# Performance work log

Measured on AMD Instinct MI355X. Metric: run time of the kernel, lower is better.

Reference implementation:

```python
import jax, jax.numpy as jnp
import numpy as np

D_MODEL = 1024
NUM_HEADS = 16
HEAD_DIM = D_MODEL // NUM_HEADS
B, S = 4, 2048


def setup_inputs() -> dict:
    key = jax.random.key(0)
    ks = jax.random.split(key, 12)
    s = 1.0 / np.sqrt(D_MODEL)
    return {
        "inputs_q": jax.random.normal(ks[0], (B, S, D_MODEL), jnp.float32),
        "inputs_k": jax.random.normal(ks[1], (B, S, D_MODEL), jnp.float32),
        "inputs_v": jax.random.normal(ks[2], (B, S, D_MODEL), jnp.float32),
        "Wq": jax.random.normal(ks[3], (D_MODEL, D_MODEL), jnp.float32) * s,
        "bq": jax.random.normal(ks[4], (D_MODEL,), jnp.float32) * 0.01,
        "Wk": jax.random.normal(ks[5], (D_MODEL, D_MODEL), jnp.float32) * s,
        "bk": jax.random.normal(ks[6], (D_MODEL,), jnp.float32) * 0.01,
        "Wv": jax.random.normal(ks[7], (D_MODEL, D_MODEL), jnp.float32) * s,
        "bv": jax.random.normal(ks[8], (D_MODEL,), jnp.float32) * 0.01,
        "Wo": jax.random.normal(ks[9], (D_MODEL, D_MODEL), jnp.float32) * s,
        "bo": jax.random.normal(ks[10], (D_MODEL,), jnp.float32) * 0.01,
    }


def reference(inputs_q, inputs_k, inputs_v, Wq, bq, Wk, bk, Wv, bv, Wo, bo):
    b, s, _ = inputs_q.shape
    # linear projections
    q = inputs_q @ Wq + bq  # [b, s, d_model]
    k = inputs_k @ Wk + bk
    v = inputs_v @ Wv + bv
    # split heads: bsd -> bhsd
    q = q.reshape(b, s, NUM_HEADS, HEAD_DIM).transpose(0, 2, 1, 3)
    k = k.reshape(b, s, NUM_HEADS, HEAD_DIM).transpose(0, 2, 1, 3)
    v = v.reshape(b, s, NUM_HEADS, HEAD_DIM).transpose(0, 2, 1, 3)
    scale = 1.0 / jnp.sqrt(jnp.asarray(HEAD_DIM, q.dtype))
    scores = jnp.einsum('bhqd,bhkd->bhqk', q, k) * scale  # [b,h,s,s]
    # causal mask: position q attends to k <= q
    causal = jnp.tril(jnp.ones((s, s), dtype=bool))
    scores = jnp.where(causal[None, None], scores, jnp.asarray(-jnp.inf, scores.dtype))
    attn = jax.nn.softmax(scores, axis=-1)
    ctx = jnp.einsum('bhqk,bhkd->bhqd', attn, v)  # [b,h,s,hd]
    ctx = ctx.transpose(0, 2, 1, 3).reshape(b, s, D_MODEL)
    return ctx @ Wo + bo
```

## Files before the change

kernel.cpp:

```cpp
#include <hip/hip_runtime.h>
#include <math.h>
#include <type_traits>

typedef __bf16 bf16;
typedef __attribute__((ext_vector_type(8))) __bf16 bf16x8;
typedef __attribute__((ext_vector_type(4))) float f32x4;
typedef __attribute__((ext_vector_type(16))) float f32x16;

#define SEQ 2048
#define DM 1024
#define NH 16
#define HD 64
#define BATCH 4

#define NEG_BIG (-1e30f)
#define SCALE_L2E 0.18033688011f

__device__ inline bf16x8 cvt_f32x8(const float* p) {
  f32x4 x0 = *(const f32x4*)p;
  f32x4 x1 = *(const f32x4*)(p + 4);
  bf16x8 r;
  r[0] = (bf16)x0[0]; r[1] = (bf16)x0[1]; r[2] = (bf16)x0[2]; r[3] = (bf16)x0[3];
  r[4] = (bf16)x1[0]; r[5] = (bf16)x1[1]; r[6] = (bf16)x1[2]; r[7] = (bf16)x1[3];
  return r;
}

__device__ inline void async_copy16(const bf16* g, bf16* l) {
  __builtin_amdgcn_global_load_lds(
      (const __attribute__((address_space(1))) unsigned int*)g,
      (__attribute__((address_space(3))) unsigned int*)l, 16, 0, 0);
}

__global__ __launch_bounds__(256) void cvt_kernel(const float* __restrict__ src,
                                                  bf16* __restrict__ dst) {
  size_t i = ((size_t)blockIdx.x * 256 + threadIdx.x) * 8;
  *(bf16x8*)(dst + i) = cvt_f32x8(src + i);
}

__global__ __launch_bounds__(256) void transpose_w_kernel(
    const float* __restrict__ Wq, const float* __restrict__ Wk,
    const float* __restrict__ Wv, const float* __restrict__ Wo,
    bf16* __restrict__ Tq, bf16* __restrict__ Tk,
    bf16* __restrict__ Tv, bf16* __restrict__ To) {
  __shared__ bf16 tile[64 * 66];
  int z = blockIdx.z;
  const float* src = (z == 0) ? Wq : (z == 1) ? Wk : (z == 2) ? Wv : Wo;
  bf16* dst = (z == 0) ? Tq : (z == 1) ? Tk : (z == 2) ? Tv : To;
  int n0 = blockIdx.x * 64, k0 = blockIdx.y * 64;
  int t = threadIdx.x;
  int c = t & 63, rr = t >> 6;
#pragma unroll
  for (int i = 0; i < 16; i++) {
    int k = i * 4 + rr;
    tile[k * 66 + c] = (bf16)src[(size_t)(k0 + k) * DM + n0 + c];
  }
  __syncthreads();
#pragma unroll
  for (int i = 0; i < 16; i++) {
    int n = i * 4 + rr;
    dst[(size_t)(n0 + n) * DM + k0 + c] = tile[c * 66 + n];
  }
}

__global__ __launch_bounds__(256) void transpose_v_kernel(
    const bf16* __restrict__ Vc, bf16* __restrict__ Vt) {
  __shared__ bf16 tile[64 * 66];
  int s0 = blockIdx.x * 64;
  int bh = blockIdx.y;
  int t = threadIdx.x;
  int c = t & 63, rr = t >> 6;
  const bf16* src = Vc + (size_t)bh * SEQ * HD;
  bf16* dst = Vt + (size_t)bh * HD * SEQ;
#pragma unroll
  for (int i = 0; i < 16; i++) {
    int s = i * 4 + rr;
    tile[s * 66 + c] = src[(size_t)(s0 + s) * HD + c];
  }
  __syncthreads();
#pragma unroll
  for (int i = 0; i < 16; i++) {
    int d = i * 4 + rr;
    dst[(size_t)d * SEQ + s0 + c] = tile[c * 66 + d];
  }
}

template <typename CT, int MODE>
__global__ __launch_bounds__(256) void gemm_bias_kernel(
    const bf16* __restrict__ A, const bf16* __restrict__ Bt,
    const float* __restrict__ bias, CT* __restrict__ C) {
  __shared__ bf16 As[128 * 32];
  __shared__ bf16 Bs[128 * 32];
  int m0 = blockIdx.x * 128, n0 = blockIdx.y * 128;
  int t = threadIdx.x;
  int wave = t >> 6, lane = t & 63, lr = lane & 15, lq = lane >> 4;
  int wm = (wave & 1) * 64, wn = (wave >> 1) * 64;

  f32x4 acc[4][4];
#pragma unroll
  for (int i = 0; i < 4; i++)
#pragma unroll
    for (int j = 0; j < 4; j++) acc[i][j] = (f32x4){0.f, 0.f, 0.f, 0.f};

  int srow = wave * 32 + (lane >> 2);
  int skc = lane & 3;
  const bf16* gA0 = A + (size_t)(m0 + srow) * DM + skc * 8;
  const bf16* gA1 = gA0 + (size_t)16 * DM;
  const bf16* gB0 = Bt + (size_t)(n0 + srow) * DM + skc * 8;
  const bf16* gB1 = gB0 + (size_t)16 * DM;
  bf16* lA0 = &As[(wave * 128) * 8];
  bf16* lA1 = &As[(wave * 128 + 64) * 8];
  bf16* lB0 = &Bs[(wave * 128) * 8];
  bf16* lB1 = &Bs[(wave * 128 + 64) * 8];

  for (int k0 = 0; k0 < DM; k0 += 32) {
    async_copy16(gA0, lA0);
    async_copy16(gA1, lA1);
    async_copy16(gB0, lB0);
    async_copy16(gB1, lB1);
    gA0 += 32; gA1 += 32; gB0 += 32; gB1 += 32;
    __syncthreads();

    bf16x8 af[4], bfr[4];
#pragma unroll
    for (int i = 0; i < 4; i++)
      af[i] = *(const bf16x8*)&As[(wm + i * 16 + lr) * 32 + lq * 8];
#pragma unroll
    for (int j = 0; j < 4; j++)
      bfr[j] = *(const bf16x8*)&Bs[(wn + j * 16 + lr) * 32 + lq * 8];
#pragma unroll
    for (int i = 0; i < 4; i++)
#pragma unroll
      for (int j = 0; j < 4; j++)
        acc[i][j] = __builtin_amdgcn_mfma_f32_16x16x32_bf16(af[i], bfr[j],
                                                            acc[i][j], 0, 0, 0);
    __syncthreads();
  }

#pragma unroll
  for (int j = 0; j < 4; j++) {
    int col = n0 + wn + j * 16 + lr;
    float bv = bias[col];
#pragma unroll
    for (int i = 0; i < 4; i++) {
      int row0 = m0 + wm + i * 16 + lq * 4;
#pragma unroll
      for (int r = 0; r < 4; r++) {
        int row = row0 + r;
        float v = acc[i][j][r] + bv;
        if constexpr (MODE == 0) {
          C[(size_t)row * DM + col] = (CT)v;
        } else {
          int b = row >> 11, s = row & 2047, h = col >> 6, d = col & 63;
          C[((size_t)(b * NH + h) * SEQ + s) * HD + d] = (CT)v;
        }
      }
    }
  }
}

__global__ __launch_bounds__(256, 2) void attention_kernel(
    const bf16* __restrict__ Qc, const bf16* __restrict__ Kc,
    const bf16* __restrict__ Vt, bf16* __restrict__ ctx) {
  int h = blockIdx.y, b = blockIdx.z;
  int t = threadIdx.x, wave = t >> 6, lane = t & 63;
  int l31 = lane & 31, hh = lane >> 5;
  int p = blockIdx.x * 4 + wave;

  const bf16* Qb = Qc + (size_t)(b * NH + h) * SEQ * HD;
  const bf16* Kb = Kc + (size_t)(b * NH + h) * SEQ * HD;
  const bf16* Vb = Vt + (size_t)(b * NH + h) * HD * SEQ;
  bf16* Cb = ctx + (size_t)b * SEQ * DM + h * HD;

#pragma unroll 1
  for (int pass = 0; pass < 2; pass++) {
    int tq = pass ? (63 - p) : p;
    int q0 = tq * 32;

    bf16x8 qf[4];
#pragma unroll
    for (int st = 0; st < 4; st++)
      qf[st] = *(const bf16x8*)&Qb[(size_t)(q0 + l31) * HD + st * 16 + hh * 8];

    f32x16 o[2];
#pragma unroll
    for (int dt = 0; dt < 2; dt++)
#pragma unroll
      for (int r = 0; r < 16; r++) o[dt][r] = 0.f;
    float m_st = NEG_BIG, l_st = 0.f;

    int nch = (tq >> 1) + 1;
#pragma unroll 1
    for (int c = 0; c < nch; c++) {
      int kv0 = c * 64;
      bf16x8 kf[2][4];
#pragma unroll
      for (int kt = 0; kt < 2; kt++)
#pragma unroll
        for (int st = 0; st < 4; st++)
          kf[kt][st] = *(const bf16x8*)&Kb[(size_t)(kv0 + kt * 32 + l31) * HD +
                                           st * 16 + hh * 8];
      bf16x8 vf[2][4];
#pragma unroll
      for (int dt = 0; dt < 2; dt++)
#pragma unroll
        for (int ks = 0; ks < 4; ks++)
          vf[dt][ks] = *(const bf16x8*)&Vb[(size_t)(dt * 32 + l31) * SEQ + kv0 +
                                           ks * 16 + hh * 8];

      f32x16 s[2];
#pragma unroll
      for (int kt = 0; kt < 2; kt++) {
        f32x16 acc;
#pragma unroll
        for (int r = 0; r < 16; r++) acc[r] = 0.f;
#pragma unroll
        for (int st = 0; st < 4; st++)
          acc = __builtin_amdgcn_mfma_f32_32x32x16_bf16(kf[kt][st], qf[st],
                                                        acc, 0, 0, 0);
        s[kt] = acc;
      }

      bool diag = (c == nch - 1);
      if (diag) {
        int q_g = q0 + l31;
#pragma unroll
        for (int kt = 0; kt < 2; kt++)
#pragma unroll
          for (int r = 0; r < 16; r++) {
            int key = kv0 + kt * 32 + (r & 3) + 8 * (r >> 2) + 4 * hh;
            float v = s[kt][r] * SCALE_L2E;
            s[kt][r] = (key > q_g) ? NEG_BIG : v;
          }
      } else {
#pragma unroll
        for (int kt = 0; kt < 2; kt++)
#pragma unroll
          for (int r = 0; r < 16; r++) s[kt][r] *= SCALE_L2E;
      }

      float mx = s[0][0];
#pragma unroll
      for (int r = 1; r < 16; r++) mx = fmaxf(mx, s[0][r]);
#pragma unroll
      for (int r = 0; r < 16; r++) mx = fmaxf(mx, s[1][r]);
      mx = fmaxf(mx, __shfl_xor(mx, 32));
      float mnew = fmaxf(m_st, mx);
      float alpha = exp2f(m_st - mnew);
      m_st = mnew;
      float rs = 0.f;
#pragma unroll
      for (int kt = 0; kt < 2; kt++)
#pragma unroll
        for (int r = 0; r < 16; r++) {
          float pv = exp2f(s[kt][r] - mnew);
          s[kt][r] = pv;
          rs += pv;
        }
      rs += __shfl_xor(rs, 32);
      l_st = l_st * alpha + rs;
#pragma unroll
      for (int dt = 0; dt < 2; dt++)
#pragma unroll
        for (int r = 0; r < 16; r++) o[dt][r] *= alpha;

      unsigned int W[2][8];
#pragma unroll
      for (int kt = 0; kt < 2; kt++)
#pragma unroll
        for (int w = 0; w < 8; w++) {
          unsigned int u;
          asm("v_cvt_pk_bf16_f32 %0, %1, %2"
              : "=v"(u)
              : "v"(s[kt][2 * w]), "v"(s[kt][2 * w + 1]));
          W[kt][w] = u;
        }
      bf16x8 pf[4];
#pragma unroll
      for (int kt = 0; kt < 2; kt++) {
        unsigned int x1 = hh ? W[kt][0] : W[kt][2];
        unsigned int x2 = hh ? W[kt][1] : W[kt][3];
        unsigned int x3 = hh ? W[kt][4] : W[kt][6];
        unsigned int x4 = hh ? W[kt][5] : W[kt][7];
        unsigned int y1 = (unsigned int)__shfl_xor((int)x1, 32);
        unsigned int y2 = (unsigned int)__shfl_xor((int)x2, 32);
        unsigned int y3 = (unsigned int)__shfl_xor((int)x3, 32);
        unsigned int y4 = (unsigned int)__shfl_xor((int)x4, 32);
        unsigned int* f0 = (unsigned int*)&pf[2 * kt];
        unsigned int* f1 = (unsigned int*)&pf[2 * kt + 1];
        f0[0] = hh ? y1 : W[kt][0];
        f0[1] = hh ? y2 : W[kt][1];
        f0[2] = hh ? W[kt][2] : y1;
        f0[3] = hh ? W[kt][3] : y2;
        f1[0] = hh ? y3 : W[kt][4];
        f1[1] = hh ? y4 : W[kt][5];
        f1[2] = hh ? W[kt][6] : y3;
        f1[3] = hh ? W[kt][7] : y4;
      }

#pragma unroll
      for (int dt = 0; dt < 2; dt++)
#pragma unroll
        for (int ks = 0; ks < 4; ks++)
          o[dt] = __builtin_amdgcn_mfma_f32_32x32x16_bf16(vf[dt][ks], pf[ks],
                                                          o[dt], 0, 0, 0);
    }

    float inv = 1.f / l_st;
    int row = q0 + l31;
#pragma unroll
    for (int dt = 0; dt < 2; dt++)
#pragma unroll
      for (int r = 0; r < 16; r += 2) {
        float va = o[dt][r] * inv;
        float vb = o[dt][r + 1] * inv;
        unsigned int u;
        asm("v_cvt_pk_bf16_f32 %0, %1, %2" : "=v"(u) : "v"(va), "v"(vb));
        int d = dt * 32 + (r & 3) + 8 * (r >> 2) + 4 * hh;
        *(unsigned int*)&Cb[(size_t)row * DM + d] = u;
      }
  }
}

extern "C" void kernel_launch(void* const* d_in, const int* in_sizes, int n_in,
                              void* d_out, int out_size, void* d_ws,
                              size_t ws_size, hipStream_t stream) {
  const float* iq = (const float*)d_in[0];
  const float* ik = (const float*)d_in[1];
  const float* iv = (const float*)d_in[2];
  const float* Wq = (const float*)d_in[3];
  const float* bq = (const float*)d_in[4];
  const float* Wk = (const float*)d_in[5];
  const float* bk = (const float*)d_in[6];
  const float* Wv = (const float*)d_in[7];
  const float* bv = (const float*)d_in[8];
  const float* Wo = (const float*)d_in[9];
  const float* bo = (const float*)d_in[10];

  char* ws = (char*)d_ws;
  const size_t MB = 1024 * 1024;
  bf16* Tq = (bf16*)(ws + 0 * MB);
  bf16* Tk = (bf16*)(ws + 2 * MB);
  bf16* Tv = (bf16*)(ws + 4 * MB);
  bf16* To = (bf16*)(ws + 6 * MB);
  bf16* Qc = (bf16*)(ws + 8 * MB);
  bf16* Kc = (bf16*)(ws + 24 * MB);
  bf16* Vc = (bf16*)(ws + 40 * MB);
  bf16* X = (bf16*)d_out;
  bf16* Vtp = (bf16*)d_out;
  bf16* Cx = Vc;

  transpose_w_kernel<<<dim3(16, 16, 4), 256, 0, stream>>>(Wq, Wk, Wv, Wo, Tq,
                                                          Tk, Tv, To);
  cvt_kernel<<<dim3(4096), 256, 0, stream>>>(iq, X);
  gemm_bias_kernel<bf16, 1><<<dim3(64, 8), 256, 0, stream>>>(X, Tq, bq, Qc);
  cvt_kernel<<<dim3(4096), 256, 0, stream>>>(ik, X);
  gemm_bias_kernel<bf16, 1><<<dim3(64, 8), 256, 0, stream>>>(X, Tk, bk, Kc);
  cvt_kernel<<<dim3(4096), 256, 0, stream>>>(iv, X);
  gemm_bias_kernel<bf16, 1><<<dim3(64, 8), 256, 0, stream>>>(X, Tv, bv, Vc);
  transpose_v_kernel<<<dim3(32, 64), 256, 0, stream>>>(Vc, Vtp);
  attention_kernel<<<dim3(8, 16, 4), 256, 0, stream>>>(Qc, Kc, Vtp, Cx);
  gemm_bias_kernel<float, 0><<<dim3(64, 8), 256, 0, stream>>>(Cx, To, bo,
                                                              (float*)d_out);
}
```

Before: 401.3 us.

## Double-buffer GEMM LDS, fuse V transpose into projection, remap attention blocks, add setprio

The GEMM now stages K-tiles into two LDS buffers so the next tile's async copy overlaps the current MFMAs, and drops one barrier per iteration. The V projection writes its output already transposed (a new MODE 2), which removes the separate transpose_v kernel and one round trip through memory. Attention uses a 1D grid remapped so that blocks sharing a (b,h) land on the same XCD for L2 reuse. s_setprio raises wave priority around the MFMA sections. The transposed V store writes with a stride of SEQ, so it is poorly coalesced.

```diff
diff --git a/kernel.cpp b/kernel.cpp
--- a/kernel.cpp
+++ b/kernel.cpp
@@ -62,34 +62,12 @@
   }
 }
 
-__global__ __launch_bounds__(256) void transpose_v_kernel(
-    const bf16* __restrict__ Vc, bf16* __restrict__ Vt) {
-  __shared__ bf16 tile[64 * 66];
-  int s0 = blockIdx.x * 64;
-  int bh = blockIdx.y;
-  int t = threadIdx.x;
-  int c = t & 63, rr = t >> 6;
-  const bf16* src = Vc + (size_t)bh * SEQ * HD;
-  bf16* dst = Vt + (size_t)bh * HD * SEQ;
-#pragma unroll
-  for (int i = 0; i < 16; i++) {
-    int s = i * 4 + rr;
-    tile[s * 66 + c] = src[(size_t)(s0 + s) * HD + c];
-  }
-  __syncthreads();
-#pragma unroll
-  for (int i = 0; i < 16; i++) {
-    int d = i * 4 + rr;
-    dst[(size_t)d * SEQ + s0 + c] = tile[c * 66 + d];
-  }
-}
-
 template <typename CT, int MODE>
 __global__ __launch_bounds__(256) void gemm_bias_kernel(
     const bf16* __restrict__ A, const bf16* __restrict__ Bt,
     const float* __restrict__ bias, CT* __restrict__ C) {
-  __shared__ bf16 As[128 * 32];
-  __shared__ bf16 Bs[128 * 32];
+  __shared__ bf16 As[2][128 * 32];
+  __shared__ bf16 Bs[2][128 * 32];
   int m0 = blockIdx.x * 128, n0 = blockIdx.y * 128;
   int t = threadIdx.x;
   int wave = t >> 6, lane = t & 63, lr = lane & 15, lq = lane >> 4;
@@ -107,33 +85,40 @@
   const bf16* gA1 = gA0 + (size_t)16 * DM;
   const bf16* gB0 = Bt + (size_t)(n0 + srow) * DM + skc * 8;
   const bf16* gB1 = gB0 + (size_t)16 * DM;
-  bf16* lA0 = &As[(wave * 128) * 8];
-  bf16* lA1 = &As[(wave * 128 + 64) * 8];
-  bf16* lB0 = &Bs[(wave * 128) * 8];
-  bf16* lB1 = &Bs[(wave * 128 + 64) * 8];
-
+  int oA0 = (wave * 128) * 8;
+  int oA1 = (wave * 128 + 64) * 8;
+
+  auto stage = [&](int buf) {
+    async_copy16(gA0, &As[buf][oA0]);
+    async_copy16(gA1, &As[buf][oA1]);
+    async_copy16(gB0, &Bs[buf][oA0]);
+    async_copy16(gB1, &Bs[buf][oA1]);
+    gA0 += 32; gA1 += 32; gB0 += 32; gB1 += 32;
+  };
+
+  stage(0);
+  __syncthreads();
+  int cur = 0;
   for (int k0 = 0; k0 < DM; k0 += 32) {
-    async_copy16(gA0, lA0);
-    async_copy16(gA1, lA1);
-    async_copy16(gB0, lB0);
-    async_copy16(gB1, lB1);
-    gA0 += 32; gA1 += 32; gB0 += 32; gB1 += 32;
-    __syncthreads();
+    if (k0 + 32 < DM) stage(cur ^ 1);
 
     bf16x8 af[4], bfr[4];
 #pragma unroll
     for (int i = 0; i < 4; i++)
-      af[i] = *(const bf16x8*)&As[(wm + i * 16 + lr) * 32 + lq * 8];
+      af[i] = *(const bf16x8*)&As[cur][(wm + i * 16 + lr) * 32 + lq * 8];
 #pragma unroll
     for (int j = 0; j < 4; j++)
-      bfr[j] = *(const bf16x8*)&Bs[(wn + j * 16 + lr) * 32 + lq * 8];
+      bfr[j] = *(const bf16x8*)&Bs[cur][(wn + j * 16 + lr) * 32 + lq * 8];
+    __builtin_amdgcn_s_setprio(1);
 #pragma unroll
     for (int i = 0; i < 4; i++)
 #pragma unroll
       for (int j = 0; j < 4; j++)
         acc[i][j] = __builtin_amdgcn_mfma_f32_16x16x32_bf16(af[i], bfr[j],
                                                             acc[i][j], 0, 0, 0);
+    __builtin_amdgcn_s_setprio(0);
     __syncthreads();
+    cur ^= 1;
   }
 
 #pragma unroll
@@ -149,9 +134,12 @@
         float v = acc[i][j][r] + bv;
         if constexpr (MODE == 0) {
           C[(size_t)row * DM + col] = (CT)v;
+        } else if constexpr (MODE == 1) {
+          int b = row >> 11, s = row & 2047, h = col >> 6, d = col & 63;
+          C[((size_t)(b * NH + h) * SEQ + s) * HD + d] = (CT)v;
         } else {
           int b = row >> 11, s = row & 2047, h = col >> 6, d = col & 63;
-          C[((size_t)(b * NH + h) * SEQ + s) * HD + d] = (CT)v;
+          C[((size_t)(b * NH + h) * HD + d) * SEQ + s] = (CT)v;
         }
       }
     }
@@ -161,10 +149,15 @@
 __global__ __launch_bounds__(256, 2) void attention_kernel(
     const bf16* __restrict__ Qc, const bf16* __restrict__ Kc,
     const bf16* __restrict__ Vt, bf16* __restrict__ ctx) {
-  int h = blockIdx.y, b = blockIdx.z;
   int t = threadIdx.x, wave = t >> 6, lane = t & 63;
   int l31 = lane & 31, hh = lane >> 5;
-  int p = blockIdx.x * 4 + wave;
+
+  int bid = blockIdx.x;
+  int xcd = bid & 7, qq = bid >> 3;
+  int g = xcd + 8 * (qq & 7);
+  int bx = qq >> 3;
+  int h = g & 15, b = g >> 4;
+  int p = bx * 4 + wave;
 
   const bf16* Qb = Qc + (size_t)(b * NH + h) * SEQ * HD;
   const bf16* Kb = Kc + (size_t)(b * NH + h) * SEQ * HD;
@@ -208,6 +201,7 @@
                                            ks * 16 + hh * 8];
 
       f32x16 s[2];
+      __builtin_amdgcn_s_setprio(1);
 #pragma unroll
       for (int kt = 0; kt < 2; kt++) {
         f32x16 acc;
@@ -219,6 +213,7 @@
                                                         acc, 0, 0, 0);
         s[kt] = acc;
       }
+      __builtin_amdgcn_s_setprio(0);
 
       bool diag = (c == nch - 1);
       if (diag) {
@@ -297,12 +292,14 @@
         f1[3] = hh ? W[kt][7] : y4;
       }
 
+      __builtin_amdgcn_s_setprio(1);
 #pragma unroll
       for (int dt = 0; dt < 2; dt++)
 #pragma unroll
         for (int ks = 0; ks < 4; ks++)
           o[dt] = __builtin_amdgcn_mfma_f32_32x32x16_bf16(vf[dt][ks], pf[ks],
                                                           o[dt], 0, 0, 0);
+      __builtin_amdgcn_s_setprio(0);
     }
 
     float inv = 1.f / l_st;
@@ -344,10 +341,9 @@
   bf16* To = (bf16*)(ws + 6 * MB);
   bf16* Qc = (bf16*)(ws + 8 * MB);
   bf16* Kc = (bf16*)(ws + 24 * MB);
-  bf16* Vc = (bf16*)(ws + 40 * MB);
-  bf16* X = (bf16*)d_out;
+  bf16* X = (bf16*)(ws + 40 * MB);
   bf16* Vtp = (bf16*)d_out;
-  bf16* Cx = Vc;
+  bf16* Cx = (bf16*)(ws + 40 * MB);
 
   transpose_w_kernel<<<dim3(16, 16, 4), 256, 0, stream>>>(Wq, Wk, Wv, Wo, Tq,
                                                           Tk, Tv, To);
@@ -356,9 +352,8 @@
   cvt_kernel<<<dim3(4096), 256, 0, stream>>>(ik, X);
   gemm_bias_kernel<bf16, 1><<<dim3(64, 8), 256, 0, stream>>>(X, Tk, bk, Kc);
   cvt_kernel<<<dim3(4096), 256, 0, stream>>>(iv, X);
-  gemm_bias_kernel<bf16, 1><<<dim3(64, 8), 256, 0, stream>>>(X, Tv, bv, Vc);
-  transpose_v_kernel<<<dim3(32, 64), 256, 0, stream>>>(Vc, Vtp);
-  attention_kernel<<<dim3(8, 16, 4), 256, 0, stream>>>(Qc, Kc, Vtp, Cx);
+  gemm_bias_kernel<bf16, 2><<<dim3(64, 8), 256, 0, stream>>>(X, Tv, bv, Vtp);
+  attention_kernel<<<dim3(512), 256, 0, stream>>>(Qc, Kc, Vtp, Cx);
   gemm_bias_kernel<float, 0><<<dim3(64, 8), 256, 0, stream>>>(Cx, To, bo,
                                                               (float*)d_out);
 }
```

Result: no change. 395.6 us (-1.4%).
